# Performance work log

Hardware: AMD Instinct MI355X
Metric: run time of the kernel (lower is better)

The kernel has to match this reference:

```python
import jax, jax.numpy as jnp
from jax import lax
import numpy as np

DN = ('NCHW', 'OIHW', 'NCHW')
NUM_CLASSES = 80
TOPK = 100
EPS = 1e-6


def seek_local_maximum(x, eps=EPS):
    # x: [b, c, h, w]; 8-neighbor local-max with zero padding, like the torch code
    xp = jnp.pad(x, ((0, 0), (0, 0), (1, 1), (1, 1)))
    m = ((x >= xp[:, :, :-2, 1:-1]) & (x >= xp[:, :, 2:, 1:-1])
         & (x >= xp[:, :, 1:-1, :-2]) & (x >= xp[:, :, 1:-1, 2:])
         & (x >= xp[:, :, :-2, :-2]) & (x >= xp[:, :, :-2, 2:])
         & (x >= xp[:, :, 2:, :-2]) & (x >= xp[:, :, 2:, 2:])
         & (x >= eps))
    return m.astype(x.dtype)


def setup_inputs() -> dict:
    key = jax.random.key(0)
    k1, k2, k3, k4 = jax.random.split(key, 4)
    b, c, h, w = 8, 256, 100, 152
    nc1 = NUM_CLASSES + 1
    x = jax.random.normal(k1, (b, c, h, w), dtype=jnp.float32)
    pos_embeddings = jax.random.normal(k2, (1, c, h, w), dtype=jnp.float32)
    w1 = jax.random.normal(k3, (c, c, 3, 3), dtype=jnp.float32) * 0.02
    b1 = jnp.zeros((c,), dtype=jnp.float32)
    w2 = jax.random.normal(k4, (nc1, c, 1, 1), dtype=jnp.float32) * 0.02
    b2 = jnp.zeros((nc1,), dtype=jnp.float32)
    return {"x": x, "pos_embeddings": pos_embeddings, "w1": w1, "b1": b1, "w2": w2, "b2": b2}


def reference(x, pos_embeddings, w1, b1, w2, b2):
    b, c, h, w = x.shape
    # conv 3x3 + relu + conv 1x1 -> class logits [b, nc+1, h, w]
    hid = lax.conv_general_dilated(x, w1, (1, 1), 'SAME', dimension_numbers=DN)
    hid = jax.nn.relu(hid + b1[None, :, None, None])
    logits = lax.conv_general_dilated(hid, w2, (1, 1), 'SAME', dimension_numbers=DN)
    logits = logits + b2[None, :, None, None]
    probs = jax.nn.softmax(logits, axis=1)
    # one-hot of argmax over foreground classes (excluding last 'no-object' channel)
    cls_idx = jnp.argmax(probs[:, :-1], axis=1)                    # [b, h, w]
    one_hot = jax.nn.one_hot(cls_idx, NUM_CLASSES + 1, dtype=probs.dtype)  # [b, h, w, nc+1]
    probs = probs * jnp.transpose(one_hot, (0, 3, 1, 2))
    probs = probs + seek_local_maximum(probs)
    # per-pixel foreground score, topk over spatial positions
    scores = jnp.max(probs[:, :-1], axis=1).reshape(b, h * w)      # [b, h*w]
    _, topk_idx = lax.top_k(scores, TOPK)                          # [b, topk]
    idx = topk_idx[:, None, :]                                     # [b, 1, topk]
    topk_proposals = jnp.take_along_axis(x.reshape(b, c, h * w), idx, axis=2)
    pos = jnp.broadcast_to(pos_embeddings, (b, c, h, w)).reshape(b, c, h * w)
    topk_pos_embeddings = jnp.take_along_axis(pos, idx, axis=2)
    # eval mode: topk_locations is None in the torch module; omit it
    return (topk_proposals, topk_pos_embeddings, logits)
```

## Files before the change

kernel.cpp:

```cpp
#include <hip/hip_runtime.h>
#include <hip/hip_bf16.h>

#define Hh    100
#define Ww    152
#define Pp    15200
#define Cc    256
#define NBATCH 8
#define NC1   81
#define NCLS  80
#define KTOP  100

#define PROWS 102
#define PCOLS 154
#define PIXB  1024
#define XT_BATCH_BYTES ((size_t)PROWS * PCOLS * PIXB)

typedef __attribute__((ext_vector_type(8))) short  bf16x8;
typedef __attribute__((ext_vector_type(4))) float  f32x4;

__device__ __forceinline__ unsigned short bf16_bits(float v) {
    __hip_bfloat16 h = __float2bfloat16(v);
    return *(unsigned short*)&h;
}
__device__ __forceinline__ float bf16_back(float v) {
    __hip_bfloat16 h = __float2bfloat16(v);
    return __bfloat162float(h);
}

typedef __attribute__((address_space(1))) const void GV;
typedef __attribute__((address_space(3))) void LV;
__device__ __forceinline__ void gload_lds16(const void* g, void* l) {
    __builtin_amdgcn_global_load_lds((GV*)g, (LV*)l, 16, 0, 0);
}

__global__ void pack_w(const float* __restrict__ w1, unsigned short* __restrict__ wpk)
{
    int id = blockIdx.x * 256 + threadIdx.x;
    int k = id >> 8, c = id & 255;
#pragma unroll
    for (int t = 0; t < 9; ++t) {
        float v = w1[(size_t)(k * 256 + c) * 9 + t];
        unsigned short hi = bf16_bits(v);
        unsigned short lo = bf16_bits(v - bf16_back(v));
        int region = ((c >> 5) * 9 + t) * 2;
        int base   = region * 8192;
        int pos    = (k >> 4) * 512 + ((c >> 3) & 3) * 128 + (k & 15) * 8 + (c & 7);
        wpk[base + pos]        = hi;
        wpk[base + 8192 + pos] = lo;
    }
}

__global__ __launch_bounds__(256)
void pack_x(const float* __restrict__ x, unsigned short* __restrict__ xT)
{
    __shared__ float ls[64][257];
    const int tid   = threadIdx.x;
    const int chunk = blockIdx.x;
    const int row   = blockIdx.y;
    const int n     = blockIdx.z;
    const int c0    = chunk * 64;
    const int yy    = row - 1;
    const bool rowok = ((unsigned)yy < (unsigned)Hh);

    const int lanec = tid & 63;
    const int xx    = c0 + lanec - 1;
    const bool colok = ((unsigned)xx < (unsigned)Ww);
    const bool ok = rowok && colok;

    const size_t rbase = ((size_t)n * Cc) * Pp + (size_t)(rowok ? yy : 0) * Ww
                       + (size_t)(colok ? xx : 0);
#pragma unroll 4
    for (int i = 0; i < 64; ++i) {
        const int c = (tid >> 6) + i * 4;
        float v = 0.f;
        if (ok) v = x[rbase + (size_t)c * Pp];
        ls[lanec][c] = v;
    }
    __syncthreads();

    const int cch = tid;
#pragma unroll 1
    for (int j = 0; j < 64; ++j) {
        const int pc = c0 + j;
        if (pc >= PCOLS) break;
        float v = ls[j][cch];
        unsigned short hi = bf16_bits(v);
        unsigned short lo = bf16_bits(v - bf16_back(v));
        size_t dst = (((size_t)n * PROWS + row) * PCOLS + pc) * 512 + cch;
        xT[dst]       = hi;
        xT[dst + 256] = lo;
    }
}

#define BBUFB 49152

__global__ __launch_bounds__(512, 2)
void conv3x3_mfma(const unsigned short* __restrict__ xT,
                  const unsigned short* __restrict__ wpk,
                  const float* __restrict__ b1, float* __restrict__ hid)
{
    __shared__ f32x4 ldsbuf[6144];
    char* L = (char*)ldsbuf;

    const int tid  = threadIdx.x;
    const int lane = tid & 63;
    const int wv   = tid >> 6;
    const int wm   = wv >> 2;
    const int wn   = wv & 3;
    const int quad = lane >> 4, lq = lane & 15;

    const int hwflat  = blockIdx.x + 65 * (blockIdx.y + 2 * blockIdx.z);
    const int logical = (hwflat & 7) * 130 + (hwflat >> 3);
    const int n   = logical / 130;
    const int rem = logical - n * 130;
    const int bx  = rem >> 1;
    const int k0b = rem & 1;

    const int rb = bx / 5, cb = bx - rb * 5;
    const int y0 = rb * 8;
    const int x0 = cb * 32;
    const int k0 = k0b * 128;

    const char* xb = (const char*)xT + (size_t)n * XT_BATCH_BYTES;
    const char* abase = (const char*)wpk + (size_t)(k0 >> 4) * 1024
                      + (size_t)(wm * 4) * 1024 + (size_t)lane * 16;

    const unsigned kslot = (lane & 7) ^ (lane >> 3);
    const size_t chnbase = (kslot < 4) ? (size_t)(kslot * 16)
                                       : (size_t)(448 + kslot * 16);

    auto stageB = [&](int s) {
        char* bdst = L + (size_t)(s & 1) * BBUFB;
        const size_t chn = (size_t)s * 64 + chnbase;
#pragma unroll
        for (int k6 = 0; k6 < 6; ++k6) {
            const int j   = wv + 8 * k6;
            const int pix = 8 * j + (lane >> 3);
            const int r   = pix / 34;
            const int c   = pix - r * 34;
            int prow = y0 + r; prow = prow < 102 ? prow : 101;
            const char* g = xb + (((size_t)(prow * 154 + x0 + c)) << 10) + chn;
            gload_lds16(g, bdst + (size_t)j * 1024);
        }
    };

    auto loadA = [&](int u, bf16x8 (&ah)[4], bf16x8 (&al)[4]) {
        const char* p0 = abase + (size_t)u * 32768;
#pragma unroll
        for (int m = 0; m < 4; ++m) {
            ah[m] = *(const bf16x8*)(p0 + m * 1024);
            al[m] = *(const bf16x8*)(p0 + m * 1024 + 16384);
        }
    };

    const int pix0 = wn * 2 * 34 + lq;
    auto readB = [&](int s, int t, bf16x8 (&bh)[4], bf16x8 (&bl)[4]) {
        const char* Bb = L + (size_t)(s & 1) * BBUFB;
        const int ty = t / 3, tx = t - ty * 3;
        const int pb0 = pix0 + ty * 34 + tx;
#pragma unroll
        for (int i = 0; i < 4; ++i) {
            const int pix = pb0 + (i >> 1) * 34 + (i & 1) * 16;
            const int a = pix * 128 + ((quad ^ (pix & 7)) << 4);
            bh[i] = *(const bf16x8*)(Bb + a);
            bl[i] = *(const bf16x8*)(Bb + (a ^ 64));
        }
    };

    f32x4 acc[4][4];
#pragma unroll
    for (int a = 0; a < 4; ++a)
#pragma unroll
        for (int b = 0; b < 4; ++b) acc[a][b] = 0;

    auto mfma48 = [&](bf16x8 (&ah)[4], bf16x8 (&al)[4],
                      bf16x8 (&bh)[4], bf16x8 (&bl)[4]) {
        __builtin_amdgcn_s_setprio(1);
#pragma unroll
        for (int m = 0; m < 4; ++m)
#pragma unroll
            for (int i = 0; i < 4; ++i)
                acc[m][i] = __builtin_amdgcn_mfma_f32_16x16x32_bf16(ah[m], bh[i], acc[m][i], 0, 0, 0);
#pragma unroll
        for (int m = 0; m < 4; ++m)
#pragma unroll
            for (int i = 0; i < 4; ++i)
                acc[m][i] = __builtin_amdgcn_mfma_f32_16x16x32_bf16(ah[m], bl[i], acc[m][i], 0, 0, 0);
#pragma unroll
        for (int m = 0; m < 4; ++m)
#pragma unroll
            for (int i = 0; i < 4; ++i)
                acc[m][i] = __builtin_amdgcn_mfma_f32_16x16x32_bf16(al[m], bh[i], acc[m][i], 0, 0, 0);
        __builtin_amdgcn_s_setprio(0);
    };

    bf16x8 ah[2][4], al[2][4], bh[2][4], bl[2][4];

    stageB(0);
    __syncthreads();
    loadA(0, ah[0], al[0]);
    readB(0, 0, bh[0], bl[0]);

#pragma unroll 1
    for (int s = 0; s < 8; ++s) {
        if (s < 7) stageB(s + 1);
#pragma unroll
        for (int t = 0; t < 9; ++t) {
            const int cur = t & 1, nx = cur ^ 1;
            if (t < 8) {
                loadA(s * 9 + t + 1, ah[nx], al[nx]);
                readB(s, t + 1, bh[nx], bl[nx]);
            }
            __builtin_amdgcn_sched_barrier(0);
            mfma48(ah[cur], al[cur], bh[cur], bl[cur]);
            __builtin_amdgcn_sched_barrier(0);
        }
        __syncthreads();
        if (s < 7) {
            loadA((s + 1) * 9, ah[0], al[0]);
            readB(s + 1, 0, bh[0], bl[0]);
        }
    }

#pragma unroll
    for (int m = 0; m < 4; ++m) {
        const int kb = k0 + wm * 64 + m * 16 + quad * 4;
        const float b0 = b1[kb], b1v = b1[kb + 1], b2v = b1[kb + 2], b3v = b1[kb + 3];
#pragma unroll
        for (int i = 0; i < 4; ++i) {
            const int y = y0 + wn * 2 + (i >> 1);
            const int xcol = x0 + (i & 1) * 16 + lq;
            if (y < Hh && xcol < Ww) {
                float* hp = hid + ((size_t)n * Cc + kb) * Pp + y * Ww + xcol;
                hp[0]              = fmaxf(acc[m][i].x + b0,  0.f);
                hp[Pp]             = fmaxf(acc[m][i].y + b1v, 0.f);
                hp[2 * Pp]         = fmaxf(acc[m][i].z + b2v, 0.f);
                hp[3 * (size_t)Pp] = fmaxf(acc[m][i].w + b3v, 0.f);
            }
        }
    }
}

__global__ __launch_bounds__(256, 2)
void conv1x1_softmax(const float* __restrict__ hid, const float* __restrict__ w2,
                     const float* __restrict__ b2, float* __restrict__ logits,
                     float* __restrict__ pmap, int* __restrict__ cmap)
{
    __shared__ float w2s[64 * 84];
    const int tid = threadIdx.x;
    const int p   = blockIdx.x * 256 + tid;
    const int n   = blockIdx.y;
    const bool valid = (p < Pp);
    const int psafe = valid ? p : 0;

    float acc[84];
#pragma unroll
    for (int j = 0; j < 84; ++j) acc[j] = 0.f;

#pragma unroll 1
    for (int c0 = 0; c0 < Cc; c0 += 64) {
        __syncthreads();
#pragma unroll
        for (int i = 0; i < 21; ++i) {
            int q  = i * 256 + tid;
            int cl = q / 84;
            int j  = q - cl * 84;
            float v = 0.f;
            if (j < NC1) v = w2[j * 256 + c0 + cl];
            w2s[cl * 84 + j] = v;
        }
        __syncthreads();

        const float* hptr = hid + ((size_t)n * Cc + c0) * Pp + psafe;
#pragma unroll 2
        for (int cl = 0; cl < 64; ++cl) {
            float h = hptr[(size_t)cl * Pp];
            const float4* wrow = (const float4*)(&w2s[cl * 84]);
#pragma unroll
            for (int f = 0; f < 21; ++f) {
                float4 wv = wrow[f];
                acc[f * 4 + 0] = fmaf(wv.x, h, acc[f * 4 + 0]);
                acc[f * 4 + 1] = fmaf(wv.y, h, acc[f * 4 + 1]);
                acc[f * 4 + 2] = fmaf(wv.z, h, acc[f * 4 + 2]);
                acc[f * 4 + 3] = fmaf(wv.w, h, acc[f * 4 + 3]);
            }
        }
    }

    if (valid) {
#pragma unroll
        for (int j = 0; j < NC1; ++j) acc[j] += b2[j];

        float* lp = logits + (size_t)n * NC1 * Pp + p;
#pragma unroll
        for (int j = 0; j < NC1; ++j) lp[(size_t)j * Pp] = acc[j];

        float m = -3.4e38f;
#pragma unroll
        for (int j = 0; j < NC1; ++j) m = fmaxf(m, acc[j]);
        float s = 0.f;
#pragma unroll
        for (int j = 0; j < NC1; ++j) s += __expf(acc[j] - m);
        float best = -3.4e38f; int bi = 0;
#pragma unroll
        for (int j = 0; j < NCLS; ++j) {
            if (acc[j] > best) { best = acc[j]; bi = j; }
        }
        pmap[n * Pp + p] = __expf(best - m) / s;
        cmap[n * Pp + p] = bi;
    }
}

__global__ void local_score(const float* __restrict__ pmap, const int* __restrict__ cmap,
                            float* __restrict__ scores)
{
    int p = blockIdx.x * 256 + threadIdx.x;
    int n = blockIdx.y;
    if (p >= Pp) return;
    int base = n * Pp;
    float pv = pmap[base + p];
    int   c  = cmap[base + p];
    int y = p / Ww, xc = p - y * Ww;
    bool ok = (pv >= 1e-6f);
#pragma unroll
    for (int dy = -1; dy <= 1; ++dy)
#pragma unroll
        for (int dx = -1; dx <= 1; ++dx) {
            if (dy == 0 && dx == 0) continue;
            int yy = y + dy, xx = xc + dx;
            if (yy >= 0 && yy < Hh && xx >= 0 && xx < Ww) {
                int q = base + yy * Ww + xx;
                if (cmap[q] == c && pmap[q] > pv) ok = false;
            }
        }
    scores[base + p] = pv + (ok ? 1.f : 0.f);
}

__global__ __launch_bounds__(1024)
void topk_gather(const float* __restrict__ scores, const float* __restrict__ x,
                 const float* __restrict__ pos, float* __restrict__ oprop,
                 float* __restrict__ opos)
{
    __shared__ float sv[Pp];
    __shared__ int sidx[KTOP];
    __shared__ unsigned long long red[16];
    __shared__ unsigned long long bcast;
    const int tid = threadIdx.x;
    const int n   = blockIdx.x;

    for (int i = tid; i < Pp; i += 1024) sv[i] = scores[n * Pp + i];
    __syncthreads();

    auto scan = [&]() -> unsigned long long {
        unsigned long long best = 0ull;
#pragma unroll
        for (int k = 0; k < 15; ++k) {
            const int i = tid + k * 1024;
            if (i < Pp) {
                unsigned fb = __float_as_uint(sv[i]);
                unsigned long long key =
                    ((unsigned long long)fb << 32) | (unsigned)(0xFFFF - i);
                best = key > best ? key : best;
            }
        }
        return best;
    };

    unsigned long long mybest = scan();

    for (int it = 0; it < KTOP; ++it) {
        unsigned long long b = mybest;
#pragma unroll
        for (int off = 32; off > 0; off >>= 1) {
            unsigned long long o = __shfl_down(b, off, 64);
            b = o > b ? o : b;
        }
        if ((tid & 63) == 0) red[tid >> 6] = b;
        __syncthreads();
        if (tid == 0) {
            unsigned long long bf = red[0];
#pragma unroll
            for (int w = 1; w < 16; ++w) bf = red[w] > bf ? red[w] : bf;
            int idx = 0xFFFF - (int)(bf & 0xFFFFFFFFull);
            sidx[it] = idx;
            sv[idx]  = 0.f;
            bcast    = bf;
        }
        __syncthreads();
        const unsigned long long w = bcast;
        const int idx = 0xFFFF - (int)(w & 0xFFFFFFFFull);
        if ((idx & 1023) == tid) mybest = scan();
    }

    for (int t = tid; t < Cc * KTOP; t += 1024) {
        int c = t / KTOP;
        int i = t - c * KTOP;
        int idx = sidx[i];
        oprop[n * Cc * KTOP + c * KTOP + i] = x[((size_t)n * Cc + c) * Pp + idx];
        opos [n * Cc * KTOP + c * KTOP + i] = pos[(size_t)c * Pp + idx];
    }
}

extern "C" void kernel_launch(void* const* d_in, const int* in_sizes, int n_in,
                              void* d_out, int out_size, void* d_ws, size_t ws_size,
                              hipStream_t stream)
{
    const float* x   = (const float*)d_in[0];
    const float* pos = (const float*)d_in[1];
    const float* w1  = (const float*)d_in[2];
    const float* b1  = (const float*)d_in[3];
    const float* w2  = (const float*)d_in[4];
    const float* b2  = (const float*)d_in[5];

    float* out    = (float*)d_out;
    float* oprop  = out;
    float* oposE  = out + (size_t)NBATCH * Cc * KTOP;
    float* logits = out + (size_t)2 * NBATCH * Cc * KTOP;

    unsigned short* wpk = (unsigned short*)logits;

    float* ws  = (float*)d_ws;
    float* hid = ws;
    unsigned short* xT = (unsigned short*)(ws + (size_t)NBATCH * Cc * Pp);
    char* after_xt = (char*)xT + (size_t)NBATCH * XT_BATCH_BYTES;
    float* pmap   = (float*)after_xt;
    int*   cmap   = (int*)(pmap + (size_t)NBATCH * Pp);
    float* scores = (float*)(cmap + (size_t)NBATCH * Pp);

    pack_w<<<256, 256, 0, stream>>>(w1, wpk);
    pack_x<<<dim3(3, PROWS, NBATCH), 256, 0, stream>>>(x, xT);
    conv3x3_mfma<<<dim3(65, 2, NBATCH), 512, 0, stream>>>(
        xT, wpk, b1, hid);
    conv1x1_softmax<<<dim3((Pp + 255) / 256, NBATCH), 256, 0, stream>>>(
        hid, w2, b2, logits, pmap, cmap);
    local_score<<<dim3((Pp + 255) / 256, NBATCH), 256, 0, stream>>>(
        pmap, cmap, scores);
    topk_gather<<<NBATCH, 1024, 0, stream>>>(scores, x, pos, oprop, oposE);
}
```

Measured before the change: 1.136 ms.

## Interleave A/B fragment loads with MFMA chunks and pre-transpose w2 for conv1x1

The 3x3 conv main loop is rewritten so that the hi/lo A global loads and the hi/lo B LDS reads for the next tap are split into four pieces. Each piece is interleaved between chunks of 12 MFMAs under sched barriers, and the stage loop is unrolled by two so LDS buffer parity is resolved at compile time. The intent is to hide load latency behind matrix work instead of issuing every load before one large MFMA block. Separately, w2 is transposed once into a workspace buffer so the 1x1 conv reads weights through uniform global loads, replacing LDS staging and block barriers, with a two-deep prefetch of hid. The pack_x tail loop is also unrolled. These changes add a small kernel launch and more code size, and may raise register pressure.

```diff
diff --git a/kernel.cpp b/kernel.cpp
--- a/kernel.cpp
+++ b/kernel.cpp
@@ -50,6 +50,14 @@
     }
 }
 
+__global__ void pack_w2t(const float* __restrict__ w2, float* __restrict__ w2t)
+{
+    int j = blockIdx.x;
+    int c = threadIdx.x;
+    float v = (j < NC1) ? w2[j * 256 + c] : 0.f;
+    w2t[c * 84 + j] = v;
+}
+
 __global__ __launch_bounds__(256)
 void pack_x(const float* __restrict__ x, unsigned short* __restrict__ xT)
 {
@@ -79,10 +87,10 @@
     __syncthreads();
 
     const int cch = tid;
-#pragma unroll 1
-    for (int j = 0; j < 64; ++j) {
+    const int jmax = (c0 + 64 <= PCOLS) ? 64 : (PCOLS - c0);
+#pragma unroll 4
+    for (int j = 0; j < jmax; ++j) {
         const int pc = c0 + j;
-        if (pc >= PCOLS) break;
         float v = ls[j][cch];
         unsigned short hi = bf16_bits(v);
         unsigned short lo = bf16_bits(v - bf16_back(v));
@@ -93,6 +101,38 @@
 }
 
 #define BBUFB 49152
+
+#define MM(P,M,I,CUR) acc[M][I] = __builtin_amdgcn_mfma_f32_16x16x32_bf16( \
+    (P)==2 ? al[CUR][M] : ah[CUR][M], (P)==1 ? bl[CUR][I] : bh[CUR][I], acc[M][I], 0, 0, 0);
+
+#define CH0(C) MM(0,0,0,C) MM(0,0,1,C) MM(0,0,2,C) MM(0,0,3,C) MM(0,1,0,C) MM(0,1,1,C) \
+               MM(0,1,2,C) MM(0,1,3,C) MM(0,2,0,C) MM(0,2,1,C) MM(0,2,2,C) MM(0,2,3,C)
+#define CH1(C) MM(0,3,0,C) MM(0,3,1,C) MM(0,3,2,C) MM(0,3,3,C) MM(1,0,0,C) MM(1,0,1,C) \
+               MM(1,0,2,C) MM(1,0,3,C) MM(1,1,0,C) MM(1,1,1,C) MM(1,1,2,C) MM(1,1,3,C)
+#define CH2(C) MM(1,2,0,C) MM(1,2,1,C) MM(1,2,2,C) MM(1,2,3,C) MM(1,3,0,C) MM(1,3,1,C) \
+               MM(1,3,2,C) MM(1,3,3,C) MM(2,0,0,C) MM(2,0,1,C) MM(2,0,2,C) MM(2,0,3,C)
+#define CH3(C) MM(2,1,0,C) MM(2,1,1,C) MM(2,1,2,C) MM(2,1,3,C) MM(2,2,0,C) MM(2,2,1,C) \
+               MM(2,2,2,C) MM(2,2,3,C) MM(2,3,0,C) MM(2,3,1,C) MM(2,3,2,C) MM(2,3,3,C)
+
+#define SBAR __builtin_amdgcn_sched_barrier(0)
+
+#define TAP(S,T,CUR,NX) { \
+    const int U_  = (S) * 9 + (T); \
+    const int un_ = (U_ + 1 < 72) ? U_ + 1 : 71; \
+    loadAh(un_, ah[NX]); \
+    SBAR; __builtin_amdgcn_s_setprio(1); CH0(CUR) __builtin_amdgcn_s_setprio(0); SBAR; \
+    loadAl(un_, al[NX]); \
+    SBAR; __builtin_amdgcn_s_setprio(1); CH1(CUR) __builtin_amdgcn_s_setprio(0); SBAR; \
+    if ((T) < 8) readBh((S), (T) + 1, bh[NX]); \
+    SBAR; __builtin_amdgcn_s_setprio(1); CH2(CUR) __builtin_amdgcn_s_setprio(0); SBAR; \
+    if ((T) < 8) readBl((S), (T) + 1, bl[NX]); \
+    SBAR; __builtin_amdgcn_s_setprio(1); CH3(CUR) __builtin_amdgcn_s_setprio(0); SBAR; \
+}
+
+#define TAPS_EVEN(S) TAP(S,0,0,1) TAP(S,1,1,0) TAP(S,2,0,1) TAP(S,3,1,0) TAP(S,4,0,1) \
+                     TAP(S,5,1,0) TAP(S,6,0,1) TAP(S,7,1,0) TAP(S,8,0,1)
+#define TAPS_ODD(S)  TAP(S,0,1,0) TAP(S,1,0,1) TAP(S,2,1,0) TAP(S,3,0,1) TAP(S,4,1,0) \
+                     TAP(S,5,0,1) TAP(S,6,1,0) TAP(S,7,0,1) TAP(S,8,1,0)
 
 __global__ __launch_bounds__(512, 2)
 void conv3x3_mfma(const unsigned short* __restrict__ xT,
@@ -144,17 +184,19 @@
         }
     };
 
-    auto loadA = [&](int u, bf16x8 (&ah)[4], bf16x8 (&al)[4]) {
+    auto loadAh = [&](int u, bf16x8 (&a)[4]) {
         const char* p0 = abase + (size_t)u * 32768;
 #pragma unroll
-        for (int m = 0; m < 4; ++m) {
-            ah[m] = *(const bf16x8*)(p0 + m * 1024);
-            al[m] = *(const bf16x8*)(p0 + m * 1024 + 16384);
-        }
+        for (int m = 0; m < 4; ++m) a[m] = *(const bf16x8*)(p0 + m * 1024);
+    };
+    auto loadAl = [&](int u, bf16x8 (&a)[4]) {
+        const char* p0 = abase + (size_t)u * 32768 + 16384;
+#pragma unroll
+        for (int m = 0; m < 4; ++m) a[m] = *(const bf16x8*)(p0 + m * 1024);
     };
 
     const int pix0 = wn * 2 * 34 + lq;
-    auto readB = [&](int s, int t, bf16x8 (&bh)[4], bf16x8 (&bl)[4]) {
+    auto readBh = [&](int s, int t, bf16x8 (&b)[4]) {
         const char* Bb = L + (size_t)(s & 1) * BBUFB;
         const int ty = t / 3, tx = t - ty * 3;
         const int pb0 = pix0 + ty * 34 + tx;
@@ -162,8 +204,18 @@
         for (int i = 0; i < 4; ++i) {
             const int pix = pb0 + (i >> 1) * 34 + (i & 1) * 16;
             const int a = pix * 128 + ((quad ^ (pix & 7)) << 4);
-            bh[i] = *(const bf16x8*)(Bb + a);
-            bl[i] = *(const bf16x8*)(Bb + (a ^ 64));
+            b[i] = *(const bf16x8*)(Bb + a);
+        }
+    };
+    auto readBl = [&](int s, int t, bf16x8 (&b)[4]) {
+        const char* Bb = L + (size_t)(s & 1) * BBUFB;
+        const int ty = t / 3, tx = t - ty * 3;
+        const int pb0 = pix0 + ty * 34 + tx;
+#pragma unroll
+        for (int i = 0; i < 4; ++i) {
+            const int pix = pb0 + (i >> 1) * 34 + (i & 1) * 16;
+            const int a = (pix * 128 + ((quad ^ (pix & 7)) << 4)) ^ 64;
+            b[i] = *(const bf16x8*)(Bb + a);
         }
     };
 
@@ -172,54 +224,25 @@
     for (int a = 0; a < 4; ++a)
 #pragma unroll
         for (int b = 0; b < 4; ++b) acc[a][b] = 0;
-
-    auto mfma48 = [&](bf16x8 (&ah)[4], bf16x8 (&al)[4],
-                      bf16x8 (&bh)[4], bf16x8 (&bl)[4]) {
-        __builtin_amdgcn_s_setprio(1);
-#pragma unroll
-        for (int m = 0; m < 4; ++m)
-#pragma unroll
-            for (int i = 0; i < 4; ++i)
-                acc[m][i] = __builtin_amdgcn_mfma_f32_16x16x32_bf16(ah[m], bh[i], acc[m][i], 0, 0, 0);
-#pragma unroll
-        for (int m = 0; m < 4; ++m)
-#pragma unroll
-            for (int i = 0; i < 4; ++i)
-                acc[m][i] = __builtin_amdgcn_mfma_f32_16x16x32_bf16(ah[m], bl[i], acc[m][i], 0, 0, 0);
-#pragma unroll
-        for (int m = 0; m < 4; ++m)
-#pragma unroll
-            for (int i = 0; i < 4; ++i)
-                acc[m][i] = __builtin_amdgcn_mfma_f32_16x16x32_bf16(al[m], bh[i], acc[m][i], 0, 0, 0);
-        __builtin_amdgcn_s_setprio(0);
-    };
 
     bf16x8 ah[2][4], al[2][4], bh[2][4], bl[2][4];
 
     stageB(0);
     __syncthreads();
-    loadA(0, ah[0], al[0]);
-    readB(0, 0, bh[0], bl[0]);
+    loadAh(0, ah[0]); loadAl(0, al[0]);
+    readBh(0, 0, bh[0]); readBl(0, 0, bl[0]);
 
 #pragma unroll 1
-    for (int s = 0; s < 8; ++s) {
-        if (s < 7) stageB(s + 1);
-#pragma unroll
-        for (int t = 0; t < 9; ++t) {
-            const int cur = t & 1, nx = cur ^ 1;
-            if (t < 8) {
-                loadA(s * 9 + t + 1, ah[nx], al[nx]);
-                readB(s, t + 1, bh[nx], bl[nx]);
-            }
-            __builtin_amdgcn_sched_barrier(0);
-            mfma48(ah[cur], al[cur], bh[cur], bl[cur]);
-            __builtin_amdgcn_sched_barrier(0);
-        }
+    for (int sp = 0; sp < 4; ++sp) {
+        const int s0 = sp * 2, s1 = s0 + 1;
+        stageB(s0 + 1);
+        TAPS_EVEN(s0)
         __syncthreads();
-        if (s < 7) {
-            loadA((s + 1) * 9, ah[0], al[0]);
-            readB(s + 1, 0, bh[0], bl[0]);
-        }
+        readBh(s1, 0, bh[1]); readBl(s1, 0, bl[1]);
+        if (s1 < 7) stageB(s1 + 1);
+        TAPS_ODD(s1)
+        __syncthreads();
+        if (s1 < 7) { readBh(s1 + 1, 0, bh[0]); readBl(s1 + 1, 0, bl[0]); }
     }
 
 #pragma unroll
@@ -242,11 +265,10 @@
 }
 
 __global__ __launch_bounds__(256, 2)
-void conv1x1_softmax(const float* __restrict__ hid, const float* __restrict__ w2,
+void conv1x1_softmax(const float* __restrict__ hid, const float* __restrict__ w2t,
                      const float* __restrict__ b2, float* __restrict__ logits,
                      float* __restrict__ pmap, int* __restrict__ cmap)
 {
-    __shared__ float w2s[64 * 84];
     const int tid = threadIdx.x;
     const int p   = blockIdx.x * 256 + tid;
     const int n   = blockIdx.y;
@@ -257,34 +279,18 @@
 #pragma unroll
     for (int j = 0; j < 84; ++j) acc[j] = 0.f;
 
+    const float* hptr = hid + ((size_t)n * Cc) * Pp + psafe;
+
+    float h0 = hptr[0];
+    float h1 = hptr[(size_t)Pp];
 #pragma unroll 1
-    for (int c0 = 0; c0 < Cc; c0 += 64) {
-        __syncthreads();
-#pragma unroll
-        for (int i = 0; i < 21; ++i) {
-            int q  = i * 256 + tid;
-            int cl = q / 84;
-            int j  = q - cl * 84;
-            float v = 0.f;
-            if (j < NC1) v = w2[j * 256 + c0 + cl];
-            w2s[cl * 84 + j] = v;
-        }
-        __syncthreads();
-
-        const float* hptr = hid + ((size_t)n * Cc + c0) * Pp + psafe;
-#pragma unroll 2
-        for (int cl = 0; cl < 64; ++cl) {
-            float h = hptr[(size_t)cl * Pp];
-            const float4* wrow = (const float4*)(&w2s[cl * 84]);
-#pragma unroll
-            for (int f = 0; f < 21; ++f) {
-                float4 wv = wrow[f];
-                acc[f * 4 + 0] = fmaf(wv.x, h, acc[f * 4 + 0]);
-                acc[f * 4 + 1] = fmaf(wv.y, h, acc[f * 4 + 1]);
-                acc[f * 4 + 2] = fmaf(wv.z, h, acc[f * 4 + 2]);
-                acc[f * 4 + 3] = fmaf(wv.w, h, acc[f * 4 + 3]);
-            }
-        }
+    for (int c = 0; c < Cc; ++c) {
+        const int cn = (c + 2 < Cc) ? c + 2 : Cc - 1;
+        const float hn = hptr[(size_t)cn * Pp];
+        const float* wr = w2t + c * 84;
+#pragma unroll
+        for (int j = 0; j < 84; ++j) acc[j] = fmaf(wr[j], h0, acc[j]);
+        h0 = h1; h1 = hn;
     }
 
     if (valid) {
@@ -426,13 +432,15 @@
     float* pmap   = (float*)after_xt;
     int*   cmap   = (int*)(pmap + (size_t)NBATCH * Pp);
     float* scores = (float*)(cmap + (size_t)NBATCH * Pp);
+    float* w2t    = scores + (size_t)NBATCH * Pp;
 
     pack_w<<<256, 256, 0, stream>>>(w1, wpk);
+    pack_w2t<<<84, 256, 0, stream>>>(w2, w2t);
     pack_x<<<dim3(3, PROWS, NBATCH), 256, 0, stream>>>(x, xT);
     conv3x3_mfma<<<dim3(65, 2, NBATCH), 512, 0, stream>>>(
         xT, wpk, b1, hid);
     conv1x1_softmax<<<dim3((Pp + 255) / 256, NBATCH), 256, 0, stream>>>(
-        hid, w2, b2, logits, pmap, cmap);
+        hid, w2t, b2, logits, pmap, cmap);
     local_score<<<dim3((Pp + 255) / 256, NBATCH), 256, 0, stream>>>(
         pmap, cmap, scores);
     topk_gather<<<NBATCH, 1024, 0, stream>>>(scores, x, pos, oprop, oposE);
```

New measurement: 1.117 ms. No clear change (-1.7%).
